# Performance work log

Hardware: AMD Instinct MI355X
Metric: run time of the kernel (lower is better)

Reference implementation:

```python
import jax, jax.numpy as jnp
import numpy as np

FP8_MAX = 448.0  # torch.finfo(float8_e4m3fn).max
TINY = float(np.finfo(np.float32).tiny)
BN = BK = 128  # block sizes


def _make_fp8_weight(key, N, K):
    """Mirror _create_fp8_weight: per-128x128-block scales, fp8 quantized values."""
    w = jax.random.normal(key, (N, K), jnp.float32) * 0.01
    wb = w.reshape(N // BN, BN, K // BK, BK)
    amax = jnp.abs(wb).max(axis=(1, 3))
    scale_inv = jnp.maximum(amax / FP8_MAX, TINY)  # [N/BN, K/BK]
    wq = (wb / scale_inv[:, None, :, None]).reshape(N, K)
    wq = wq.astype(jnp.float8_e4m3fn).astype(jnp.float32)  # fp8-rounded values
    return wq, scale_inv


def _dequant(wq, scale_inv):
    N, K = wq.shape
    nb, kb = scale_inv.shape
    wb = wq.reshape(nb, N // nb, kb, K // kb) * scale_inv[:, None, :, None]
    return wb.reshape(N, K)


def setup_inputs() -> dict:
    key = jax.random.key(0)
    kx, k1, k2, k3 = jax.random.split(key, 4)
    T, H, F = 4096, 2048, 7168  # tokens, hidden_dim, ffn_dim
    x = jax.random.normal(kx, (T, H), jnp.float32)
    w1_q, w1_s = _make_fp8_weight(k1, F, H)
    w3_q, w3_s = _make_fp8_weight(k3, F, H)
    w2_q, w2_s = _make_fp8_weight(k2, H, F)
    return {"hidden_states": x, "w1_q": w1_q, "w1_s": w1_s,
            "w3_q": w3_q, "w3_s": w3_s, "w2_q": w2_q, "w2_s": w2_s}


def reference(hidden_states, w1_q, w1_s, w3_q, w3_s, w2_q, w2_s):
    x = hidden_states
    w1 = _dequant(w1_q, w1_s)  # [F, H]
    w3 = _dequant(w3_q, w3_s)  # [F, H]
    w2 = _dequant(w2_q, w2_s)  # [H, F]
    g = x @ w1.T               # [T, F]
    u = x @ w3.T               # [T, F]
    fused = jax.nn.silu(g) * u
    return fused @ w2.T        # [T, H]
```

## Files before the change

kernel.cpp:

```cpp
#include <hip/hip_runtime.h>
#include <stdint.h>

typedef __attribute__((ext_vector_type(8))) short short8;
typedef __attribute__((ext_vector_type(4))) float floatx4;

__device__ __forceinline__ unsigned short f2bf(float f) {
  union { float f; unsigned int u; } c; c.f = f;
  unsigned int u = c.u;
  unsigned int r = (u + 0x7fffu + ((u >> 16) & 1u)) >> 16;
  return (unsigned short)r;
}
__device__ __forceinline__ float bf2f(unsigned short h) {
  union { unsigned int u; float f; } c; c.u = ((unsigned int)h) << 16;
  return c.f;
}

__device__ __forceinline__ void load16_to_lds(const void* g, void* l) {
  __builtin_amdgcn_global_load_lds(
      (const __attribute__((address_space(1))) unsigned int*)g,
      (__attribute__((address_space(3))) unsigned int*)l, 16, 0, 0);
}

__global__ void f32_to_bf16_kernel(const float* __restrict__ in,
                                   unsigned short* __restrict__ out, long n4) {
  long i = blockIdx.x * (long)blockDim.x + threadIdx.x;
  if (i >= n4) return;
  float4 v = ((const float4*)in)[i];
  ushort4 o;
  o.x = f2bf(v.x); o.y = f2bf(v.y); o.z = f2bf(v.z); o.w = f2bf(v.w);
  ((ushort4*)out)[i] = o;
}

__global__ void dequant_kernel(const float* __restrict__ wq,
                               const float* __restrict__ s,
                               unsigned short* __restrict__ out,
                               int K, int sK, long n4) {
  long i = blockIdx.x * (long)blockDim.x + threadIdx.x;
  if (i >= n4) return;
  long e = i * 4;
  int n = (int)(e / K);
  int k = (int)(e - (long)n * K);
  float sc = s[(n >> 7) * sK + (k >> 7)];
  float4 v = ((const float4*)wq)[i];
  ushort4 o;
  o.x = f2bf(v.x * sc); o.y = f2bf(v.y * sc);
  o.z = f2bf(v.z * sc); o.w = f2bf(v.w * sc);
  ((ushort4*)out)[i] = o;
}

__global__ __launch_bounds__(512, 4) void dual_gemm_silu(
    const unsigned short* __restrict__ A,
    const unsigned short* __restrict__ B1,
    const unsigned short* __restrict__ B3,
    unsigned short* __restrict__ C,
    int M, int N, int K) {
  __shared__ unsigned short As[128 * 32];
  __shared__ unsigned short B1s[128 * 32];
  __shared__ unsigned short B3s[128 * 32];

  const int tid = threadIdx.x;
  const int lane = tid & 63;
  const int wave = tid >> 6;
  const int wm = wave >> 2;
  const int wn = wave & 3;
  const int m0 = blockIdx.y * 128, n0 = blockIdx.x * 128;

  const int f0 = tid * 8;
  const int ar = tid >> 2;
  const int ac = (tid & 3) * 8;

  const int q = lane >> 4;
  const int r16 = lane & 15;

  floatx4 acc_g[4][2], acc_u[4][2];
#pragma unroll
  for (int i = 0; i < 4; i++)
#pragma unroll
    for (int j = 0; j < 2; j++) {
      acc_g[i][j] = (floatx4){0.f, 0.f, 0.f, 0.f};
      acc_u[i][j] = (floatx4){0.f, 0.f, 0.f, 0.f};
    }

  const unsigned short* ag = A + (size_t)(m0 + ar) * K + ac;
  const unsigned short* b1g = B1 + (size_t)(n0 + ar) * K + ac;
  const unsigned short* b3g = B3 + (size_t)(n0 + ar) * K + ac;

  for (int k0 = 0; k0 < K; k0 += 32) {
    load16_to_lds(ag + k0, &As[f0]);
    load16_to_lds(b1g + k0, &B1s[f0]);
    load16_to_lds(b3g + k0, &B3s[f0]);
    __syncthreads();

    short8 a[4], b1[2], b3[2];
#pragma unroll
    for (int t = 0; t < 4; t++)
      a[t] = *(const short8*)&As[(wm * 64 + t * 16 + r16) * 32 + q * 8];
#pragma unroll
    for (int j = 0; j < 2; j++) {
      b1[j] = *(const short8*)&B1s[(wn * 32 + j * 16 + r16) * 32 + q * 8];
      b3[j] = *(const short8*)&B3s[(wn * 32 + j * 16 + r16) * 32 + q * 8];
    }
#pragma unroll
    for (int i = 0; i < 4; i++)
#pragma unroll
      for (int j = 0; j < 2; j++) {
        acc_g[i][j] =
            __builtin_amdgcn_mfma_f32_16x16x32_bf16(a[i], b1[j], acc_g[i][j], 0, 0, 0);
        acc_u[i][j] =
            __builtin_amdgcn_mfma_f32_16x16x32_bf16(a[i], b3[j], acc_u[i][j], 0, 0, 0);
      }
    __syncthreads();
  }

#pragma unroll
  for (int i = 0; i < 4; i++) {
    int row0 = m0 + wm * 64 + i * 16 + q * 4;
#pragma unroll
    for (int j = 0; j < 2; j++) {
      int col = n0 + wn * 32 + j * 16 + r16;
#pragma unroll
      for (int rr = 0; rr < 4; rr++) {
        float gv = acc_g[i][j][rr];
        float uv = acc_u[i][j][rr];
        float sv = gv / (1.f + __expf(-gv)) * uv;
        C[(size_t)(row0 + rr) * N + col] = f2bf(sv);
      }
    }
  }
}

__global__ __launch_bounds__(256) void gemm_nt_f32(
    const unsigned short* __restrict__ A,
    const unsigned short* __restrict__ B,
    float* __restrict__ C,
    int M, int N, int K) {
  __shared__ unsigned short As[128 * 32];
  __shared__ unsigned short Bs[128 * 32];

  const int tid = threadIdx.x;
  const int lane = tid & 63;
  const int wave = tid >> 6;
  const int wm = wave >> 1, wn = wave & 1;
  const int m0 = blockIdx.y * 128, n0 = blockIdx.x * 128;

  const int f0 = tid * 8;
  const int ar = f0 >> 5;
  const int ac = f0 & 31;

  const int q = lane >> 4;
  const int r16 = lane & 15;

  floatx4 acc[4][4];
#pragma unroll
  for (int i = 0; i < 4; i++)
#pragma unroll
    for (int j = 0; j < 4; j++) acc[i][j] = (floatx4){0.f, 0.f, 0.f, 0.f};

  const unsigned short* Abase = A + (size_t)m0 * K;
  const unsigned short* Bbase = B + (size_t)n0 * K;

  for (int k0 = 0; k0 < K; k0 += 32) {
    load16_to_lds(Abase + (size_t)ar * K + k0 + ac, &As[f0]);
    load16_to_lds(Abase + (size_t)(64 + ar) * K + k0 + ac, &As[2048 + f0]);
    load16_to_lds(Bbase + (size_t)ar * K + k0 + ac, &Bs[f0]);
    load16_to_lds(Bbase + (size_t)(64 + ar) * K + k0 + ac, &Bs[2048 + f0]);
    __syncthreads();

    short8 a[4], b[4];
#pragma unroll
    for (int t = 0; t < 4; t++) {
      a[t] = *(const short8*)&As[(wm * 64 + t * 16 + r16) * 32 + q * 8];
      b[t] = *(const short8*)&Bs[(wn * 64 + t * 16 + r16) * 32 + q * 8];
    }
#pragma unroll
    for (int i = 0; i < 4; i++)
#pragma unroll
      for (int j = 0; j < 4; j++)
        acc[i][j] =
            __builtin_amdgcn_mfma_f32_16x16x32_bf16(a[i], b[j], acc[i][j], 0, 0, 0);
    __syncthreads();
  }

#pragma unroll
  for (int i = 0; i < 4; i++) {
    int row0 = m0 + wm * 64 + i * 16 + q * 4;
#pragma unroll
    for (int j = 0; j < 4; j++) {
      int col = n0 + wn * 64 + j * 16 + r16;
#pragma unroll
      for (int rr = 0; rr < 4; rr++)
        C[(size_t)(row0 + rr) * N + col] = acc[i][j][rr];
    }
  }
}

extern "C" void kernel_launch(void* const* d_in, const int* in_sizes, int n_in,
                              void* d_out, int out_size, void* d_ws, size_t ws_size,
                              hipStream_t stream) {
  const float* x = (const float*)d_in[0];
  const float* w1q = (const float*)d_in[1];
  const float* w1s = (const float*)d_in[2];
  const float* w3q = (const float*)d_in[3];
  const float* w3s = (const float*)d_in[4];
  const float* w2q = (const float*)d_in[5];
  const float* w2s = (const float*)d_in[6];

  const int T = 4096, H = 2048, F = 7168;

  char* ws = (char*)d_ws;
  unsigned short* xb  = (unsigned short*)ws;  ws += (size_t)T * H * 2;
  unsigned short* w1b = (unsigned short*)ws;  ws += (size_t)F * H * 2;
  unsigned short* w3b = (unsigned short*)ws;  ws += (size_t)F * H * 2;
  unsigned short* g   = (unsigned short*)ws;  ws += (size_t)T * F * 2;
  unsigned short* w2b = w1b;

  long xn4 = (long)T * H / 4;
  long wn4 = (long)F * H / 4;

  f32_to_bf16_kernel<<<(xn4 + 255) / 256, 256, 0, stream>>>(x, xb, xn4);
  dequant_kernel<<<(wn4 + 255) / 256, 256, 0, stream>>>(w1q, w1s, w1b, H, H / 128, wn4);
  dequant_kernel<<<(wn4 + 255) / 256, 256, 0, stream>>>(w3q, w3s, w3b, H, H / 128, wn4);

  dual_gemm_silu<<<dim3(F / 128, T / 128), 512, 0, stream>>>(xb, w1b, w3b, g, T, F, H);

  dequant_kernel<<<(wn4 + 255) / 256, 256, 0, stream>>>(w2q, w2s, w2b, F, F / 128, wn4);
  gemm_nt_f32<<<dim3(H / 128, T / 128), 256, 0, stream>>>(g, w2b, (float*)d_out, T, H, F);
}
```

Baseline: 642.2 us.

## Fuse w1/w3 dequant, use 2D dequant grids, and switch down-proj GEMM to 8 waves

New measurement: 648.4 us. About the same (+1.0%).

```diff
diff --git a/kernel.cpp b/kernel.cpp
--- a/kernel.cpp
+++ b/kernel.cpp
@@ -31,21 +31,42 @@
   ((ushort4*)out)[i] = o;
 }
 
-__global__ void dequant_kernel(const float* __restrict__ wq,
-                               const float* __restrict__ s,
-                               unsigned short* __restrict__ out,
-                               int K, int sK, long n4) {
-  long i = blockIdx.x * (long)blockDim.x + threadIdx.x;
-  if (i >= n4) return;
-  long e = i * 4;
-  int n = (int)(e / K);
-  int k = (int)(e - (long)n * K);
+__global__ void dequant2_kernel(const float* __restrict__ w1q,
+                                const float* __restrict__ s1,
+                                const float* __restrict__ w3q,
+                                const float* __restrict__ s3,
+                                unsigned short* __restrict__ o1,
+                                unsigned short* __restrict__ o3,
+                                int K, int sK) {
+  int n = blockIdx.y;
+  int k = blockIdx.x * 1024 + threadIdx.x * 4;
+  size_t idx = (size_t)n * K + k;
+  int sidx = (n >> 7) * sK + (k >> 7);
+  float sc1 = s1[sidx], sc3 = s3[sidx];
+  float4 v1 = *(const float4*)(w1q + idx);
+  float4 v3 = *(const float4*)(w3q + idx);
+  ushort4 a, b;
+  a.x = f2bf(v1.x * sc1); a.y = f2bf(v1.y * sc1);
+  a.z = f2bf(v1.z * sc1); a.w = f2bf(v1.w * sc1);
+  b.x = f2bf(v3.x * sc3); b.y = f2bf(v3.y * sc3);
+  b.z = f2bf(v3.z * sc3); b.w = f2bf(v3.w * sc3);
+  *(ushort4*)(o1 + idx) = a;
+  *(ushort4*)(o3 + idx) = b;
+}
+
+__global__ void dequant1_kernel(const float* __restrict__ wq,
+                                const float* __restrict__ s,
+                                unsigned short* __restrict__ out,
+                                int K, int sK) {
+  int n = blockIdx.y;
+  int k = blockIdx.x * 1024 + threadIdx.x * 4;
+  size_t idx = (size_t)n * K + k;
   float sc = s[(n >> 7) * sK + (k >> 7)];
-  float4 v = ((const float4*)wq)[i];
+  float4 v = *(const float4*)(wq + idx);
   ushort4 o;
   o.x = f2bf(v.x * sc); o.y = f2bf(v.y * sc);
   o.z = f2bf(v.z * sc); o.w = f2bf(v.w * sc);
-  ((ushort4*)out)[i] = o;
+  *(ushort4*)(out + idx) = o;
 }
 
 __global__ __launch_bounds__(512, 4) void dual_gemm_silu(
@@ -129,7 +150,7 @@
   }
 }
 
-__global__ __launch_bounds__(256) void gemm_nt_f32(
+__global__ __launch_bounds__(512, 4) void gemm_nt_f32_8w(
     const unsigned short* __restrict__ A,
     const unsigned short* __restrict__ B,
     float* __restrict__ C,
@@ -140,42 +161,42 @@
   const int tid = threadIdx.x;
   const int lane = tid & 63;
   const int wave = tid >> 6;
-  const int wm = wave >> 1, wn = wave & 1;
+  const int wm = wave >> 2;
+  const int wn = wave & 3;
   const int m0 = blockIdx.y * 128, n0 = blockIdx.x * 128;
 
   const int f0 = tid * 8;
-  const int ar = f0 >> 5;
-  const int ac = f0 & 31;
+  const int ar = tid >> 2;
+  const int ac = (tid & 3) * 8;
 
   const int q = lane >> 4;
   const int r16 = lane & 15;
 
-  floatx4 acc[4][4];
+  floatx4 acc[4][2];
 #pragma unroll
   for (int i = 0; i < 4; i++)
 #pragma unroll
-    for (int j = 0; j < 4; j++) acc[i][j] = (floatx4){0.f, 0.f, 0.f, 0.f};
-
-  const unsigned short* Abase = A + (size_t)m0 * K;
-  const unsigned short* Bbase = B + (size_t)n0 * K;
+    for (int j = 0; j < 2; j++) acc[i][j] = (floatx4){0.f, 0.f, 0.f, 0.f};
+
+  const unsigned short* ag = A + (size_t)(m0 + ar) * K + ac;
+  const unsigned short* bg = B + (size_t)(n0 + ar) * K + ac;
 
   for (int k0 = 0; k0 < K; k0 += 32) {
-    load16_to_lds(Abase + (size_t)ar * K + k0 + ac, &As[f0]);
-    load16_to_lds(Abase + (size_t)(64 + ar) * K + k0 + ac, &As[2048 + f0]);
-    load16_to_lds(Bbase + (size_t)ar * K + k0 + ac, &Bs[f0]);
-    load16_to_lds(Bbase + (size_t)(64 + ar) * K + k0 + ac, &Bs[2048 + f0]);
-    __syncthreads();
-
-    short8 a[4], b[4];
-#pragma unroll
-    for (int t = 0; t < 4; t++) {
+    load16_to_lds(ag + k0, &As[f0]);
+    load16_to_lds(bg + k0, &Bs[f0]);
+    __syncthreads();
+
+    short8 a[4], b[2];
+#pragma unroll
+    for (int t = 0; t < 4; t++)
       a[t] = *(const short8*)&As[(wm * 64 + t * 16 + r16) * 32 + q * 8];
-      b[t] = *(const short8*)&Bs[(wn * 64 + t * 16 + r16) * 32 + q * 8];
-    }
+#pragma unroll
+    for (int j = 0; j < 2; j++)
+      b[j] = *(const short8*)&Bs[(wn * 32 + j * 16 + r16) * 32 + q * 8];
 #pragma unroll
     for (int i = 0; i < 4; i++)
 #pragma unroll
-      for (int j = 0; j < 4; j++)
+      for (int j = 0; j < 2; j++)
         acc[i][j] =
             __builtin_amdgcn_mfma_f32_16x16x32_bf16(a[i], b[j], acc[i][j], 0, 0, 0);
     __syncthreads();
@@ -185,8 +206,8 @@
   for (int i = 0; i < 4; i++) {
     int row0 = m0 + wm * 64 + i * 16 + q * 4;
 #pragma unroll
-    for (int j = 0; j < 4; j++) {
-      int col = n0 + wn * 64 + j * 16 + r16;
+    for (int j = 0; j < 2; j++) {
+      int col = n0 + wn * 32 + j * 16 + r16;
 #pragma unroll
       for (int rr = 0; rr < 4; rr++)
         C[(size_t)(row0 + rr) * N + col] = acc[i][j][rr];
@@ -211,18 +232,18 @@
   unsigned short* xb  = (unsigned short*)ws;  ws += (size_t)T * H * 2;
   unsigned short* w1b = (unsigned short*)ws;  ws += (size_t)F * H * 2;
   unsigned short* w3b = (unsigned short*)ws;  ws += (size_t)F * H * 2;
+  unsigned short* w2b = (unsigned short*)ws;  ws += (size_t)H * F * 2;
   unsigned short* g   = (unsigned short*)ws;  ws += (size_t)T * F * 2;
-  unsigned short* w2b = w1b;
 
   long xn4 = (long)T * H / 4;
-  long wn4 = (long)F * H / 4;
 
   f32_to_bf16_kernel<<<(xn4 + 255) / 256, 256, 0, stream>>>(x, xb, xn4);
-  dequant_kernel<<<(wn4 + 255) / 256, 256, 0, stream>>>(w1q, w1s, w1b, H, H / 128, wn4);
-  dequant_kernel<<<(wn4 + 255) / 256, 256, 0, stream>>>(w3q, w3s, w3b, H, H / 128, wn4);
+  dequant2_kernel<<<dim3(H / 1024, F), 256, 0, stream>>>(
+      w1q, w1s, w3q, w3s, w1b, w3b, H, H / 128);
+  dequant1_kernel<<<dim3(F / 1024, H), 256, 0, stream>>>(
+      w2q, w2s, w2b, F, F / 128);
 
   dual_gemm_silu<<<dim3(F / 128, T / 128), 512, 0, stream>>>(xb, w1b, w3b, g, T, F, H);
 
-  dequant_kernel<<<(wn4 + 255) / 256, 256, 0, stream>>>(w2q, w2s, w2b, F, F / 128, wn4);
-  gemm_nt_f32<<<dim3(H / 128, T / 128), 256, 0, stream>>>(g, w2b, (float*)d_out, T, H, F);
-}
+  gemm_nt_f32_8w<<<dim3(H / 128, T / 128), 512, 0, stream>>>(g, w2b, (float*)d_out, T, H, F);
+}
```
